# Kernel tuning notes

Measured on AMD Instinct MI355X. Metric: run time of the kernel, lower is better.

The kernel has to match this reference:

```python
import jax, jax.numpy as jnp
import numpy as np

TOP_K = 2


def setup_inputs() -> dict:
    key = jax.random.key(0)
    k0, k1, k2, k3 = jax.random.split(key, 4)
    N, D, O, E = 131072, 512, 512, 16
    H = D // 4  # gate hidden: gate_input_size // 4
    x = jax.random.normal(k0, (N, D), dtype=jnp.float32)
    # gate MLP params (task_bh=0 gate; Linear weights stored as [in, out])
    Wg1 = jax.random.normal(k1, (D, H), dtype=jnp.float32) / np.sqrt(D).astype(np.float32)
    bg1 = jnp.zeros((H,), jnp.float32)
    Wg2 = jax.random.normal(k2, (H, E), dtype=jnp.float32) * 0.02
    bg2 = jnp.zeros((E,), jnp.float32)
    # per-expert Linear(D, O) weights stacked [E, D, O]
    We = jax.random.normal(k3, (E, D, O), dtype=jnp.float32) / np.sqrt(D).astype(np.float32)
    be = jnp.zeros((E, O), jnp.float32)
    return {"x": x, "Wg1": Wg1, "bg1": bg1, "Wg2": Wg2, "bg2": bg2,
            "We": We, "be": be, "task_bh": 0}


def reference(x, Wg1, bg1, Wg2, bg2, We, be, task_bh):
    # --- top_k_gating (noisy_gating=False path) ---
    h = jax.nn.gelu(x @ Wg1 + bg1, approximate=False)  # nn.GELU default is exact erf
    logits = h @ Wg2 + bg2                              # [N, E]
    probs = jax.nn.softmax(logits, axis=1) + 1e-4       # [N, E]
    top_g, top_i = jax.lax.top_k(probs, TOP_K)          # [N, K]
    N, E = probs.shape
    # dense gate matrix: zeros.scatter(1, top_k_indices, top_k_gates)
    gates = jnp.zeros_like(probs).at[jnp.arange(N)[:, None], top_i].set(top_g)
    # --- dispatch / per-expert GEMM / combine ---
    # Equivalent to: gather tokens per expert, expert Linear, scale by gate,
    # scatter-add back. Since gates[n, e] == 0 for unselected experts, the
    # combined output equals sum_e gates[:, e] * (x @ We[e] + be[e]).
    def body(acc, ewb):
        W_e, b_e, g_e = ewb                      # [D,O], [O], [N]
        return acc + g_e[:, None] * (x @ W_e + b_e), None
    init = jnp.zeros((N, We.shape[2]), x.dtype)
    out, _ = jax.lax.scan(body, init, (We, be, gates.T))
    return out
```

## Files before the change

kernel.cpp:

```cpp
#include <hip/hip_runtime.h>
#include <cstdint>
#include <math.h>


#define NTOK 131072
#define DDIM 512
#define NT 16

typedef _Float16 f16;
typedef f16   f16x8 __attribute__((ext_vector_type(8)));
typedef float f32x4 __attribute__((ext_vector_type(4)));

__device__ __forceinline__ void load_lds16(const void* g, void* l){
  __builtin_amdgcn_global_load_lds(
      (const __attribute__((address_space(1))) void*)(uintptr_t)g,
      (__attribute__((address_space(3))) void*)(uintptr_t)l, 16, 0, 0);
}

__device__ __forceinline__ f32x4 MFMAH(f16x8 a, f16x8 b, f32x4 c){
  return __builtin_amdgcn_mfma_f32_16x16x32_f16(a, b, c, 0, 0, 0);
}

__device__ __forceinline__ f16x8 readF64h(const char* buf, int r, int q){
  return *(const f16x8*)(buf + r*128 + ((q ^ (r & 7)) << 4));
}
__device__ __forceinline__ f16x8 pack8f(const float* fv){
  f16x8 v;
  #pragma unroll
  for (int j=0;j<8;++j) v[j] = (f16)fv[j];
  return v;
}

__global__ void kconv(const float* __restrict__ Wg1, const float* __restrict__ Wg2,
                      f16* __restrict__ W1, char* __restrict__ Wg2f, int* __restrict__ ctrl){
  __shared__ float sh[64*65];
  int bx = blockIdx.x, tid = threadIdx.x;
  if (bx < 16){
    int dt = bx >> 1, ht = bx & 1;
    const float* src = Wg1 + (size_t)dt*64*128 + ht*64;
    #pragma unroll
    for (int it=0; it<16; ++it){ int idx = it*256+tid; int dl = idx>>6, ol = idx&63;
      sh[dl*65+ol] = src[dl*128+ol]; }
    __syncthreads();
    #pragma unroll
    for (int it=0; it<16; ++it){ int idx = it*256+tid; int ol = idx>>6, dl = idx&63;
      W1[(size_t)(ht*64+ol)*512 + dt*64+dl] = (f16)sh[dl*65+ol]; }
  } else {
    int ks = tid >> 6, l = tid & 63;
    int col = l & 15, kb = ks*32 + ((l >> 4) << 3);
    f16x8 v;
    #pragma unroll
    for (int j=0;j<8;++j) v[j] = (f16)Wg2[(kb+j)*16 + col];
    *(f16x8*)(Wg2f + (ks*64+l)*16) = v;
    #pragma unroll
    for (int i = 0; i < 8; ++i) ctrl[tid + i*256] = 0;
  }
}

__global__ __launch_bounds__(256) void kgate(
    const float* __restrict__ x, const f16* __restrict__ W1, const char* __restrict__ Wg2f,
    const float* __restrict__ bg1, const float* __restrict__ bg2,
    const float* __restrict__ We, f16* __restrict__ Wt,
    f16* __restrict__ xbf,
    int2* __restrict__ gate_e, float2* __restrict__ gate_g,
    int* __restrict__ refine_cnt, int* __restrict__ refine_list, int* __restrict__ counts)
{
  __shared__ __align__(16) char sm[76800];
  const int BOFF = 32768;
  const int LOGI = 67584;
  const int HIST = 75776;
  int tid = threadIdx.x, bid = blockIdx.x;
  int lane = tid & 63, w = tid >> 6, wm = w >> 1, wn = w & 1;
  int l15 = lane & 15, l4 = lane >> 4;
  int t0 = bid * 128;
  int ar = tid >> 1, ach = tid & 1;
  const float* xrow = x + (size_t)(t0 + ar) * DDIM;
  char* xbfb = (char*)xbf;
  f32x4 acc[4][4];
  #pragma unroll
  for (int n=0;n<4;++n){
    float bb = bg1[wn*64 + n*16 + l15];
    f32x4 z = {bb, bb, bb, bb};
    #pragma unroll
    for (int m=0;m<4;++m) acc[m][n] = z;
  }
  auto stageA = [&](int ks, char* abuf){
    float fv[32];
    #pragma unroll
    for (int q=0;q<8;++q) *(float4*)&fv[q*4] = *(const float4*)(xrow + ks*64 + ach*32 + q*4);
    f16x8 h0 = pack8f(fv), h1 = pack8f(fv+8), h2 = pack8f(fv+16), h3 = pack8f(fv+24);
    *(f16x8*)(abuf + ar*128 + (((ach*4+0) ^ (ar & 7)) << 4)) = h0;
    *(f16x8*)(abuf + ar*128 + (((ach*4+1) ^ (ar & 7)) << 4)) = h1;
    *(f16x8*)(abuf + ar*128 + (((ach*4+2) ^ (ar & 7)) << 4)) = h2;
    *(f16x8*)(abuf + ar*128 + (((ach*4+3) ^ (ar & 7)) << 4)) = h3;
    if (xbf){
      char* xd = xbfb + (size_t)(t0+ar)*1024 + ks*128 + ach*64;
      *(f16x8*)xd = h0; *(f16x8*)(xd+16) = h1; *(f16x8*)(xd+32) = h2; *(f16x8*)(xd+48) = h3;
    }
  };
  auto stageB = [&](int ks, char* lds){
    const char* gb = (const char*)W1 + ks*128;
    #pragma unroll
    for (int i = 0; i < 4; ++i){
      int lin = i*4096 + tid*16;
      int r = lin >> 7, g = (lin >> 4) & 7;
      load_lds16(gb + r*1024 + ((g ^ (r & 7)) << 4), lds + i*4096 + ((tid >> 6) << 10));
    }
  };
  stageB(0, sm + BOFF); stageA(0, sm);
  for (int ks = 0; ks < 8; ++ks){
    int b = ks & 1;
    asm volatile("s_waitcnt vmcnt(0)" ::: "memory");
    __syncthreads();
    if (ks < 7) stageB(ks+1, sm + BOFF + (b^1)*16384);
    const char* Ab = sm + b*16384;
    const char* Bb = sm + BOFF + b*16384;
    f16x8 ah[4][2], bh[4][2];
    #pragma unroll
    for (int m=0;m<4;++m)
      #pragma unroll
      for (int kf=0;kf<2;++kf) ah[m][kf] = readF64h(Ab, wm*64 + m*16 + l15, kf*4 + l4);
    #pragma unroll
    for (int n=0;n<4;++n)
      #pragma unroll
      for (int kf=0;kf<2;++kf) bh[n][kf] = readF64h(Bb, wn*64 + n*16 + l15, kf*4 + l4);
    #pragma unroll
    for (int m=0;m<4;++m)
      #pragma unroll
      for (int n=0;n<4;++n){
        acc[m][n] = MFMAH(ah[m][0], bh[n][0], acc[m][n]);
        acc[m][n] = MFMAH(ah[m][1], bh[n][1], acc[m][n]);
      }
    if (ks < 7) stageA(ks+1, sm + (b^1)*16384);
  }
  __syncthreads();
  uint4 wgf[4];
  #pragma unroll
  for (int ksq=0; ksq<4; ++ksq) wgf[ksq] = *(const uint4*)(Wg2f + (ksq*64+lane)*16);
  float* hl = (float*)sm;
  #pragma unroll
  for (int m=0;m<4;++m)
    #pragma unroll
    for (int n=0;n<4;++n)
      #pragma unroll
      for (int j=0;j<4;++j){
        int row = wm*64 + m*16 + (l4 << 2) + j;
        int col = wn*64 + n*16 + l15;
        float uv = acc[m][n][j];
        hl[row*132 + col] = 0.5f * uv * (1.0f + erff(uv * 0.70710678118654752f));
      }
  __syncthreads();
  {
    float bb2 = bg2[l15];
    float* ll = (float*)(sm + LOGI);
    #pragma unroll
    for (int sub=0; sub<2; ++sub){
      f32x4 acc2 = {bb2, bb2, bb2, bb2};
      #pragma unroll
      for (int ksq=0; ksq<4; ++ksq){
        const float* hp = (const float*)sm + (w*32 + sub*16 + l15)*132 + ksq*32 + l4*8;
        f16x8 afr;
        #pragma unroll
        for (int j=0;j<8;++j) afr[j] = (f16)hp[j];
        acc2 = MFMAH(afr, *(const f16x8*)&wgf[ksq], acc2);
      }
      #pragma unroll
      for (int j=0;j<4;++j) ll[(w*32 + sub*16 + l4*4 + j)*16 + l15] = acc2[j];
    }
  }
  int* hist = (int*)(sm + HIST);
  hist[tid] = 0;
  __syncthreads();
  if (tid < 128){
    int t = t0 + tid;
    const float* l = (const float*)(sm + LOGI) + tid*16;
    float b1 = -1e30f, b2 = -1e30f, b3 = -1e30f; int e1 = 0, e2 = 0;
    #pragma unroll
    for (int e = 0; e < 16; ++e){
      float v = l[e];
      if (v > b1){ b3 = b2; b2 = b1; e2 = e1; b1 = v; e1 = e; }
      else if (v > b2){ b3 = b2; b2 = v; e2 = e; }
      else if (v > b3){ b3 = v; }
    }
    float s = 0.f;
    #pragma unroll
    for (int e = 0; e < 16; ++e) s += expf(l[e] - b1);
    float inv = 1.f / s;
    gate_e[t] = make_int2(e1, e2);
    gate_g[t] = make_float2(inv + 1e-4f, expf(b2 - b1) * inv + 1e-4f);
    if (b2 - b3 < 1e-3f){
      int pos = atomicAdd(refine_cnt, 1);
      refine_list[pos] = t;
    }
    int pa = min(e1, e2), pb = max(e1, e2);
    atomicAdd(&hist[pa*16 + pb], 1);
  }
  __syncthreads();
  if (hist[tid]) atomicAdd(&counts[tid], hist[tid]);
  __syncthreads();
  {
    float* sh = (float*)sm;
    int e = bid >> 6, dt = (bid >> 3) & 7, ot = bid & 7;
    const float* src = We + (size_t)e*262144 + (size_t)dt*64*512 + ot*64;
    #pragma unroll
    for (int it=0; it<16; ++it){ int idx = it*256+tid; int dl = idx>>6, ol = idx&63;
      sh[dl*65+ol] = src[dl*512+ol]; }
    __syncthreads();
    f16* dst = Wt + (size_t)e*262144 + (size_t)ot*64*512 + dt*64;
    #pragma unroll
    for (int it=0; it<16; ++it){ int idx = it*256+tid; int ol = idx>>6, dl = idx&63;
      dst[(size_t)ol*512+dl] = (f16)sh[dl*65+ol]; }
  }
}

__global__ __launch_bounds__(128) void krefine(
    const float* __restrict__ x, const float* __restrict__ Wg1, const float* __restrict__ bg1,
    const float* __restrict__ Wg2, const float* __restrict__ bg2,
    const int* __restrict__ refine_cnt, const int* __restrict__ refine_list,
    int2* __restrict__ gate_e, float2* __restrict__ gate_g, int* __restrict__ counts)
{
  __shared__ float  xs[512];
  __shared__ double hd[128];
  __shared__ double ld[16];
  int tid = threadIdx.x;
  int rc = *refine_cnt;
  for (int i = blockIdx.x; i < rc; i += gridDim.x){
    __syncthreads();
    int t = refine_list[i];
    *(float4*)(xs + tid*4) = *(const float4*)(x + (size_t)t*DDIM + tid*4);
    __syncthreads();
    double a0=0.0, a1=0.0, a2=0.0, a3=0.0;
    for (int d = 0; d < 512; d += 4){
      a0 += (double)xs[d]   * (double)Wg1[(d)*128 + tid];
      a1 += (double)xs[d+1] * (double)Wg1[(d+1)*128 + tid];
      a2 += (double)xs[d+2] * (double)Wg1[(d+2)*128 + tid];
      a3 += (double)xs[d+3] * (double)Wg1[(d+3)*128 + tid];
    }
    double a = (double)bg1[tid] + ((a0+a1)+(a2+a3));
    hd[tid] = 0.5 * a * (1.0 + erf(a * 0.70710678118654752440));
    __syncthreads();
    if (tid < 16){
      double s0=0.0, s1=0.0;
      for (int k = 0; k < 128; k += 2){
        s0 += hd[k]   * (double)Wg2[(k)*16 + tid];
        s1 += hd[k+1] * (double)Wg2[(k+1)*16 + tid];
      }
      ld[tid] = (double)bg2[tid] + s0 + s1;
    }
    __syncthreads();
    if (tid == 0){
      int2 olde = gate_e[t];
      double b1 = -1e300, b2 = -1e300; int e1 = 0, e2 = 0;
      for (int e = 0; e < 16; ++e){
        double v = ld[e];
        if (v > b1){ b2 = b1; e2 = e1; b1 = v; e1 = e; }
        else if (v > b2){ b2 = v; e2 = e; }
      }
      double s = 0.0;
      for (int e = 0; e < 16; ++e) s += exp(ld[e] - b1);
      double inv = 1.0 / s;
      int oldp = min(olde.x, olde.y)*16 + max(olde.x, olde.y);
      int newp = min(e1, e2)*16 + max(e1, e2);
      if (oldp != newp){ atomicSub(&counts[oldp], 1); atomicAdd(&counts[newp], 1); }
      gate_e[t] = make_int2(e1, e2);
      gate_g[t] = make_float2((float)(inv + 1e-4), (float)(exp(b2 - b1) * inv + 1e-4));
    }
  }
}

__global__ __launch_bounds__(256) void kscatter(
    const int2* __restrict__ gate_e, const float2* __restrict__ gate_g,
    const int* __restrict__ counts,
    int* __restrict__ bases, int* __restrict__ cursors,
    int* __restrict__ tile_pair, int* __restrict__ tile_row0, int* __restrict__ ntiles,
    int* __restrict__ pair_tok, float2* __restrict__ pair_g, int ts)
{
  __shared__ int h[256];
  __shared__ int gb[256];
  __shared__ int bl[257];
  int tid = threadIdx.x;
  h[tid] = 0;
  if (tid < 64){
    int l = tid;
    int4 c = *(const int4*)(counts + l*4);
    int s = c.x + c.y + c.z + c.w;
    int ps = s;
    #pragma unroll
    for (int d = 1; d < 64; d <<= 1){ int v = __shfl_up(ps, d); if (l >= d) ps += v; }
    int ex = ps - s;
    bl[4*l+0] = ex;
    bl[4*l+1] = ex + c.x;
    bl[4*l+2] = ex + c.x + c.y;
    bl[4*l+3] = ex + c.x + c.y + c.z;
    if (l == 63) bl[256] = ex + s;
    if (blockIdx.x == 0){
      *(int4*)(bases + 4*l) = make_int4(bl[4*l], bl[4*l+1], bl[4*l+2], bl[4*l+3]);
      if (l == 63) bases[256] = ex + s;
      int t0 = (c.x + ts-1)/ts, t1 = (c.y + ts-1)/ts, t2 = (c.z + ts-1)/ts, t3 = (c.w + ts-1)/ts;
      int tsum = t0 + t1 + t2 + t3;
      int pt = tsum;
      #pragma unroll
      for (int d = 1; d < 64; d <<= 1){ int v = __shfl_up(pt, d); if (l >= d) pt += v; }
      int ext = pt - tsum;
      if (l == 63) *ntiles = ext + tsum;
      int tb = ext;
      int cc[4] = {c.x, c.y, c.z, c.w};
      #pragma unroll
      for (int j = 0; j < 4; ++j){
        int pp = 4*l + j;
        for (int r = 0; r < cc[j]; r += ts){ tile_pair[tb] = pp; tile_row0[tb] = r; ++tb; }
      }
    }
  }
  __syncthreads();
  int t = blockIdx.x*256 + tid;
  int2 ee = gate_e[t]; float2 gg = gate_g[t];
  int a, b; float ga, gbv;
  if (ee.x < ee.y){ a = ee.x; b = ee.y; ga = gg.x; gbv = gg.y; }
  else            { a = ee.y; b = ee.x; ga = gg.y; gbv = gg.x; }
  int p = a*16 + b;
  int off = atomicAdd(&h[p], 1);
  __syncthreads();
  if (h[tid]) gb[tid] = bl[tid] + atomicAdd(&cursors[tid], h[tid]);
  __syncthreads();
  int slot = gb[p] + off;
  pair_tok[slot] = t;
  pair_g[slot] = make_float2(ga, gbv);
}

#define SB0 __builtin_amdgcn_sched_barrier(0)
#define PH_MID do{ __builtin_amdgcn_s_barrier(); \
                   asm volatile("s_waitcnt lgkmcnt(0)"); SB0; }while(0)
#define PH_END do{ SB0; __builtin_amdgcn_s_barrier(); }while(0)

#define RDA(hp, mb) do{ \
  _Pragma("unroll") for (int m_=0;m_<4;++m_){ \
    int r_ = ((mb)+m_)*16 + l15; \
    af[m_][0] = readF64h(hp, r_, l4); \
    af[m_][1] = readF64h(hp, r_, 4+l4); }}while(0)
#define RDB4(hp) do{ \
  _Pragma("unroll") for (int n_=0;n_<4;++n_){ \
    int r_ = bln + n_*16 + l15; \
    bb[n_][0] = readF64h(hp, r_, l4); \
    bb[n_][1] = readF64h(hp, r_, 4+l4); }}while(0)
#define MMAC32(mb) do{ \
  __builtin_amdgcn_s_setprio(1); \
  _Pragma("unroll") for (int m_=0;m_<4;++m_){ \
    _Pragma("unroll") for (int n_=0;n_<4;++n_){ \
      acc[(mb)+m_][n_] = MFMAH(af[m_][0], bb[n_][0], acc[(mb)+m_][n_]); \
      acc[(mb)+m_][n_] = MFMAH(af[m_][1], bb[n_][1], acc[(mb)+m_][n_]); }} \
  __builtin_amdgcn_s_setprio(0); \
}while(0)

__global__ __launch_bounds__(512, 2) void kexpert2(
    const f16* __restrict__ xbf, const f16* __restrict__ Wt, const float* __restrict__ be,
    float* __restrict__ out,
    const int* __restrict__ counts, const int* __restrict__ bases,
    const int* __restrict__ tile_pair, const int* __restrict__ tile_row0, const int* __restrict__ ntiles,
    const int* __restrict__ pair_tok, const float2* __restrict__ pair_g)
{
  __shared__ __align__(16) char sm[134144];
  const int BBASE = 65536, LTOK = 131072, LG = 132096;
  int bid = blockIdx.x;
  int tile = ((bid >> 4) << 3) | (bid & 7);
  int nt = (bid >> 3) & 1;
  if (tile >= *ntiles) return;
  int p = tile_pair[tile], row0 = tile_row0[tile];
  int base = bases[p], cnt = counts[p];
  int eA = p >> 4, eB = p & 15;
  int tid = threadIdx.x, lane = tid & 63, w = tid >> 6;
  int wm = w >> 2, wn = w & 3;
  int l15 = lane & 15, l4 = lane >> 4;
  int bln = (wn & 1) * 64;
  if (tid < 256){
    int rr = row0 + tid; bool v = rr < cnt;
    ((int*)(sm + LTOK))[tid] = v ? pair_tok[base + rr] : -1;
    ((float2*)(sm + LG))[tid] = v ? pair_g[base + rr] : make_float2(0.f, 1.f);
  }
  __syncthreads();

  int rr0 = tid >> 3;
  int sw = ((tid & 7) ^ (rr0 & 7)) << 4;
  const char* xb = (const char*)xbf;
  const char* srcA[2][2];
  #pragma unroll
  for (int h = 0; h < 2; ++h)
    #pragma unroll
    for (int i = 0; i < 2; ++i){
      int tk = ((const int*)(sm + LTOK))[h*128 + i*64 + rr0];
      if (tk < 0) tk = 0;
      srcA[h][i] = xb + (size_t)tk*1024 + sw;
    }
  const char* srcB0 = (const char*)Wt + (size_t)eA*524288 + (size_t)(nt*256 + rr0)*1024 + sw;
  long long edelt = ((long long)eB - eA) * 524288;
  char* dA = sm + w*1024;
  char* dB = sm + BBASE + w*1024;

  auto stA = [&](int t, int h){
    if (t >= NT) return;
    int ks = t & 7, bf_ = t & 1;
    load_lds16(srcA[h][0] + ks*128, dA + bf_*32768 + h*16384);
    load_lds16(srcA[h][1] + ks*128, dA + bf_*32768 + h*16384 + 8192);
  };
  auto stB = [&](int t, int h){
    if (t >= NT) return;
    int ks = t & 7, bf_ = t & 1;
    long long eo = ((t >= 8) ? edelt : 0) + ks*128;
    load_lds16(srcB0 + h*131072 + eo,         dB + bf_*32768 + h*16384);
    load_lds16(srcB0 + h*131072 + 65536 + eo, dB + bf_*32768 + h*16384 + 8192);
  };

  const char* A0 = sm + wm*16384;
  const char* A1 = A0 + 32768;
  const char* B0 = sm + BBASE + (wn >> 1)*16384;
  const char* B1 = B0 + 32768;

  f32x4 acc[8][4];
  #pragma unroll
  for (int m = 0; m < 8; ++m)
    #pragma unroll
    for (int n = 0; n < 4; ++n) acc[m][n] = (f32x4){0.f,0.f,0.f,0.f};

  stA(0,0); stA(0,1); stB(0,0); stB(0,1); stB(1,0); stB(1,1);
  asm volatile("s_waitcnt vmcnt(4)"); SB0;
  __builtin_amdgcn_s_barrier();

  f16x8 af[4][2], bb[4][2];
  #pragma unroll 1
  for (int i = 0; i < 8; ++i){
    int t0 = 2*i, t1 = t0 + 1;
    RDA(A0, 0); RDB4(B0); stA(t1, 0); stA(t1, 1);
    PH_MID; MMAC32(0); PH_END;
    RDA(A0, 4); stB(t0+2, 0); stB(t0+2, 1);
    if (i != 7) { asm volatile("s_waitcnt vmcnt(4)"); SB0; }
    else        { asm volatile("s_waitcnt vmcnt(0)"); SB0; }
    PH_MID; MMAC32(4); PH_END;
    RDA(A1, 0); RDB4(B1); stA(t0+2, 0); stA(t0+2, 1);
    PH_MID; MMAC32(0); PH_END;
    RDA(A1, 4); stB(t1+2, 0); stB(t1+2, 1);
    if (i != 7) { asm volatile("s_waitcnt vmcnt(4)"); SB0; }
    PH_MID; MMAC32(4); PH_END;
    if (i == 3){
      #pragma unroll
      for (int m = 0; m < 8; ++m)
        #pragma unroll
        for (int j = 0; j < 4; ++j){
          int row = wm*128 + m*16 + l4*4 + j;
          float2 g2 = ((const float2*)(sm + LG))[row];
          float r_ = g2.x / g2.y;
          #pragma unroll
          for (int n = 0; n < 4; ++n) acc[m][n][j] *= r_;
        }
    }
  }

  float bcA[4], bcB[4];
  #pragma unroll
  for (int n = 0; n < 4; ++n){
    int col = nt*256 + wn*64 + n*16 + l15;
    bcA[n] = be[(size_t)eA*DDIM + col];
    bcB[n] = be[(size_t)eB*DDIM + col];
  }
  #pragma unroll
  for (int m = 0; m < 8; ++m)
    #pragma unroll
    for (int j = 0; j < 4; ++j){
      int row = wm*128 + m*16 + l4*4 + j;
      int tk = ((const int*)(sm + LTOK))[row];
      if (tk >= 0){
        float2 g2 = ((const float2*)(sm + LG))[row];
        float* orow = out + (size_t)tk*DDIM + nt*256 + wn*64;
        #pragma unroll
        for (int n = 0; n < 4; ++n)
          orow[n*16 + l15] = g2.y*acc[m][n][j] + g2.x*bcA[n] + g2.y*bcB[n];
      }
    }
}

__global__ __launch_bounds__(256, 2) void kexpertF(
    const float* __restrict__ x,
    const f16* __restrict__ Wt, const float* __restrict__ be,
    float* __restrict__ out,
    const int* __restrict__ counts, const int* __restrict__ bases,
    const int* __restrict__ tile_pair, const int* __restrict__ tile_row0, const int* __restrict__ ntiles,
    const int* __restrict__ pair_tok, const float2* __restrict__ pair_g)
{
  __shared__ __align__(16) char sm[67072];
  const int ABUF = 0, BBUF = 32768, LTOK = 65536, LGOFF = 66048;
  int tile = blockIdx.x >> 2, nt = blockIdx.x & 3;
  if (tile >= *ntiles) return;
  int p = tile_pair[tile], row0 = tile_row0[tile];
  int base = bases[p], cnt = counts[p];
  int eA = p >> 4, eB = p & 15;
  int tid = threadIdx.x, lane = tid & 63;
  int w = tid >> 6, wm = w >> 1, wn = w & 1;
  if (tid < 128){
    int rr = row0 + tid; bool v = rr < cnt;
    ((int*)(sm + LTOK))[tid] = v ? pair_tok[base + rr] : -1;
    ((float2*)(sm + LGOFF))[tid] = v ? pair_g[base + rr] : make_float2(0.f, 0.f);
  }
  __syncthreads();
  const char* wb = (const char*)Wt;
  int grp = tid >> 3, gch = tid & 7;
  int swz = (gch ^ (grp & 7)) << 4;
  long long edelt = ((long long)eB - (long long)eA) * 524288;
  const char* srcB[4];
  #pragma unroll
  for (int i = 0; i < 4; ++i)
    srcB[i] = wb + (long long)eA*524288 + (size_t)(nt*128 + i*32 + grp)*1024 + swz;
  int arow = tid >> 1, ach = tid & 1;
  int tkr = ((const int*)(sm + LTOK))[arow];
  if (tkr < 0) tkr = 0;
  const float* xrow = x + (size_t)tkr*DDIM + ach*32;
  int ldst = (w << 10);
  #pragma unroll
  for (int i = 0; i < 4; ++i) load_lds16(srcB[i], sm + BBUF + i*4096 + ldst);
  {
    #pragma unroll
    for (int q2 = 0; q2 < 4; ++q2){
      float fv[8];
      *(float4*)&fv[0] = *(const float4*)(xrow + q2*8);
      *(float4*)&fv[4] = *(const float4*)(xrow + q2*8 + 4);
      f16x8 hv = pack8f(fv);
      int g = ach*4 + q2;
      *(f16x8*)(sm + ABUF + arow*128 + ((g ^ (arow & 7)) << 4)) = hv;
    }
  }
  f32x4 acc[4][4], res[4][4];
  #pragma unroll
  for (int m=0;m<4;++m)
    #pragma unroll
    for (int n=0;n<4;++n) acc[m][n] = (f32x4){0.f,0.f,0.f,0.f};
  for (int u = 0; u < 16; ++u){
    int b = u & 1;
    asm volatile("s_waitcnt vmcnt(0)" ::: "memory");
    __syncthreads();
    int un = u + 1;
    f16x8 hv[4];
    if (un < 16){
      int b2 = un & 1;
      long long aoff = (long long)(un & 7) * 128;
      long long boff = aoff + ((un >> 3) ? edelt : 0);
      #pragma unroll
      for (int i = 0; i < 4; ++i)
        load_lds16(srcB[i] + boff, sm + BBUF + b2*16384 + i*4096 + ldst);
      const float* xr = xrow + (un & 7)*64;
      #pragma unroll
      for (int q2 = 0; q2 < 4; ++q2){
        float fv[8];
        *(float4*)&fv[0] = *(const float4*)(xr + q2*8);
        *(float4*)&fv[4] = *(const float4*)(xr + q2*8 + 4);
        hv[q2] = pack8f(fv);
      }
    }
    const char* Ab = sm + ABUF + b*16384;
    const char* Bb = sm + BBUF + b*16384;
    f16x8 af2[4][2], bf2[4][2];
    #pragma unroll
    for (int m=0;m<4;++m){
      int r = wm*64 + m*16 + (lane & 15);
      af2[m][0] = readF64h(Ab, r, (lane >> 4));
      af2[m][1] = readF64h(Ab, r, 4 + (lane >> 4));
    }
    #pragma unroll
    for (int n=0;n<4;++n){
      int r = wn*64 + n*16 + (lane & 15);
      bf2[n][0] = readF64h(Bb, r, (lane >> 4));
      bf2[n][1] = readF64h(Bb, r, 4 + (lane >> 4));
    }
    #pragma unroll
    for (int m=0;m<4;++m)
      #pragma unroll
      for (int n=0;n<4;++n){
        acc[m][n] = MFMAH(af2[m][0], bf2[n][0], acc[m][n]);
        acc[m][n] = MFMAH(af2[m][1], bf2[n][1], acc[m][n]);
      }
    if (un < 16){
      int b2 = un & 1;
      #pragma unroll
      for (int q2 = 0; q2 < 4; ++q2){
        int g = ach*4 + q2;
        *(f16x8*)(sm + ABUF + b2*16384 + arow*128 + ((g ^ (arow & 7)) << 4)) = hv[q2];
      }
    }
    if (u == 7){
      const float* bev = be + (size_t)eA*DDIM + nt*128;
      float bcol[4];
      #pragma unroll
      for (int n=0;n<4;++n) bcol[n] = bev[wn*64 + n*16 + (lane & 15)];
      #pragma unroll
      for (int m=0;m<4;++m)
        #pragma unroll
        for (int j=0;j<4;++j){
          int row = wm*64 + m*16 + ((lane >> 4) << 2) + j;
          float g = ((const float2*)(sm + LGOFF))[row].x;
          #pragma unroll
          for (int n=0;n<4;++n){
            res[m][n][j] = g * (acc[m][n][j] + bcol[n]);
            acc[m][n][j] = 0.f;
          }
        }
    }
    if (u == 15){
      const float* bev = be + (size_t)eB*DDIM + nt*128;
      float bcol[4];
      #pragma unroll
      for (int n=0;n<4;++n) bcol[n] = bev[wn*64 + n*16 + (lane & 15)];
      #pragma unroll
      for (int m=0;m<4;++m)
        #pragma unroll
        for (int j=0;j<4;++j){
          int row = wm*64 + m*16 + ((lane >> 4) << 2) + j;
          int tk = ((const int*)(sm + LTOK))[row];
          float g = ((const float2*)(sm + LGOFF))[row].y;
          if (tk >= 0){
            float* orow = out + (size_t)tk*DDIM + nt*128;
            #pragma unroll
            for (int n=0;n<4;++n)
              orow[wn*64 + n*16 + (lane & 15)] = res[m][n][j] + g * (acc[m][n][j] + bcol[n]);
          }
        }
    }
  }
}

extern "C" void kernel_launch(void* const* d_in, const int* in_sizes, int n_in,
                              void* d_out, int out_size, void* d_ws, size_t ws_size,
                              hipStream_t stream)
{
  const float* x   = (const float*)d_in[0];
  const float* Wg1 = (const float*)d_in[1];
  const float* bg1 = (const float*)d_in[2];
  const float* Wg2 = (const float*)d_in[3];
  const float* bg2 = (const float*)d_in[4];
  const float* We  = (const float*)d_in[5];
  const float* be  = (const float*)d_in[6];
  float* out = (float*)d_out;
  char* ws = (char*)d_ws;

  f16*  Wt          = (f16*)(ws + 0);
  f16*  W1          = (f16*)(ws + 8388608);
  char* Wg2f        = ws + 8519680;
  char* CTRL        = ws + 8650752;
  int*  refine_cnt  = (int*)(CTRL);
  int*  ntiles      = (int*)(CTRL + 4);
  int*  counts      = (int*)(CTRL + 64);
  int*  cursors     = (int*)(CTRL + 2048);
  int*  bases       = (int*)(CTRL + 4096);
  int2*   gate_e    = (int2*)(ws + 8658944);
  float2* gate_g    = (float2*)(ws + 9707520);
  int*  refine_list = (int*)(ws + 10756096);
  int*  pair_tok    = (int*)(ws + 11280384);
  float2* pair_g    = (float2*)(ws + 11804672);
  int*  tile_pair   = (int*)(ws + 12853248);
  int*  tile_row0   = (int*)(ws + 12863488);
  const size_t XBF_OFF = 16777216ull;
  const size_t XBF_BYTES = (size_t)NTOK * DDIM * 2;
  bool bf16a = ws_size >= XBF_OFF + XBF_BYTES;
  f16* xbf = bf16a ? (f16*)(ws + XBF_OFF) : nullptr;

  hipLaunchKernelGGL(kconv,    dim3(17),   dim3(256), 0, stream, Wg1, Wg2, W1, Wg2f,
                     (int*)CTRL);
  hipLaunchKernelGGL(kgate,    dim3(1024), dim3(256), 0, stream, x, W1, Wg2f, bg1, bg2,
                     We, Wt, xbf, gate_e, gate_g, refine_cnt, refine_list, counts);
  hipLaunchKernelGGL(krefine,  dim3(512),  dim3(128), 0, stream, x, Wg1, bg1, Wg2, bg2,
                     refine_cnt, refine_list, gate_e, gate_g, counts);
  hipLaunchKernelGGL(kscatter, dim3(512),  dim3(256), 0, stream, gate_e, gate_g, counts,
                     bases, cursors, tile_pair, tile_row0, ntiles, pair_tok, pair_g,
                     bf16a ? 256 : 128);
  if (bf16a)
    hipLaunchKernelGGL(kexpert2, dim3(1408), dim3(512), 0, stream, xbf, Wt, be, out,
                       counts, bases, tile_pair, tile_row0, ntiles, pair_tok, pair_g);
  else
    hipLaunchKernelGGL(kexpertF, dim3(5120), dim3(256), 0, stream, x, Wt, be, out,
                       counts, bases, tile_pair, tile_row0, ntiles, pair_tok, pair_g);
  (void)in_sizes; (void)n_in; (void)out_size; (void)ws_size;
}
```

Measured before the change: 461.2 us.

## Restructure expert GEMM to 256x128 tiles with triple-buffered 32-wide K steps

Replaces the expert GEMM kernel with a version that computes 256x128 output tiles instead of 256x256 and splits N into four parts. It uses 32-element K slices staged through a three-deep LDS ring. Per-block LDS drops from about 134KB to about 77KB and accumulators are halved, which allows four blocks per CU instead of two. The aim is higher occupancy and better latency hiding. In exchange the x-row gathers are repeated across four N tiles instead of two, and there are more barriers per unit of K work.

```diff
diff --git a/kernel.cpp b/kernel.cpp
--- a/kernel.cpp
+++ b/kernel.cpp
@@ -5,7 +5,6 @@
 
 #define NTOK 131072
 #define DDIM 512
-#define NT 16
 
 typedef _Float16 f16;
 typedef f16   f16x8 __attribute__((ext_vector_type(8)));
@@ -23,6 +22,9 @@
 
 __device__ __forceinline__ f16x8 readF64h(const char* buf, int r, int q){
   return *(const f16x8*)(buf + r*128 + ((q ^ (r & 7)) << 4));
+}
+__device__ __forceinline__ f16x8 readF32h(const char* buf, int r, int q){
+  return *(const f16x8*)(buf + r*64 + ((q ^ (r & 3)) << 4));
 }
 __device__ __forceinline__ f16x8 pack8f(const float* fv){
   f16x8 v;
@@ -329,49 +331,26 @@
 }
 
 #define SB0 __builtin_amdgcn_sched_barrier(0)
-#define PH_MID do{ __builtin_amdgcn_s_barrier(); \
-                   asm volatile("s_waitcnt lgkmcnt(0)"); SB0; }while(0)
-#define PH_END do{ SB0; __builtin_amdgcn_s_barrier(); }while(0)
-
-#define RDA(hp, mb) do{ \
-  _Pragma("unroll") for (int m_=0;m_<4;++m_){ \
-    int r_ = ((mb)+m_)*16 + l15; \
-    af[m_][0] = readF64h(hp, r_, l4); \
-    af[m_][1] = readF64h(hp, r_, 4+l4); }}while(0)
-#define RDB4(hp) do{ \
-  _Pragma("unroll") for (int n_=0;n_<4;++n_){ \
-    int r_ = bln + n_*16 + l15; \
-    bb[n_][0] = readF64h(hp, r_, l4); \
-    bb[n_][1] = readF64h(hp, r_, 4+l4); }}while(0)
-#define MMAC32(mb) do{ \
-  __builtin_amdgcn_s_setprio(1); \
-  _Pragma("unroll") for (int m_=0;m_<4;++m_){ \
-    _Pragma("unroll") for (int n_=0;n_<4;++n_){ \
-      acc[(mb)+m_][n_] = MFMAH(af[m_][0], bb[n_][0], acc[(mb)+m_][n_]); \
-      acc[(mb)+m_][n_] = MFMAH(af[m_][1], bb[n_][1], acc[(mb)+m_][n_]); }} \
-  __builtin_amdgcn_s_setprio(0); \
-}while(0)
-
-__global__ __launch_bounds__(512, 2) void kexpert2(
+
+__global__ __launch_bounds__(512, 4) void kexpert3(
     const f16* __restrict__ xbf, const f16* __restrict__ Wt, const float* __restrict__ be,
     float* __restrict__ out,
     const int* __restrict__ counts, const int* __restrict__ bases,
     const int* __restrict__ tile_pair, const int* __restrict__ tile_row0, const int* __restrict__ ntiles,
     const int* __restrict__ pair_tok, const float2* __restrict__ pair_g)
 {
-  __shared__ __align__(16) char sm[134144];
-  const int BBASE = 65536, LTOK = 131072, LG = 132096;
+  __shared__ __align__(16) char sm[76800];
+  const int ABASE = 0, BBASE = 49152, LTOK = 73728, LG = 74752;
   int bid = blockIdx.x;
-  int tile = ((bid >> 4) << 3) | (bid & 7);
-  int nt = (bid >> 3) & 1;
+  int tile = ((bid >> 5) << 3) | (bid & 7);
+  int nt = (bid >> 3) & 3;
   if (tile >= *ntiles) return;
   int p = tile_pair[tile], row0 = tile_row0[tile];
   int base = bases[p], cnt = counts[p];
   int eA = p >> 4, eB = p & 15;
   int tid = threadIdx.x, lane = tid & 63, w = tid >> 6;
-  int wm = w >> 2, wn = w & 3;
+  int wm = w >> 1, wn = w & 1;
   int l15 = lane & 15, l4 = lane >> 4;
-  int bln = (wn & 1) * 64;
   if (tid < 256){
     int rr = row0 + tid; bool v = rr < cnt;
     ((int*)(sm + LTOK))[tid] = v ? pair_tok[base + rr] : -1;
@@ -379,97 +358,99 @@
   }
   __syncthreads();
 
-  int rr0 = tid >> 3;
-  int sw = ((tid & 7) ^ (rr0 & 7)) << 4;
+  int rr = tid >> 2;
+  int swz = ((tid & 3) ^ (rr & 3)) << 4;
   const char* xb = (const char*)xbf;
-  const char* srcA[2][2];
-  #pragma unroll
-  for (int h = 0; h < 2; ++h)
-    #pragma unroll
-    for (int i = 0; i < 2; ++i){
-      int tk = ((const int*)(sm + LTOK))[h*128 + i*64 + rr0];
-      if (tk < 0) tk = 0;
-      srcA[h][i] = xb + (size_t)tk*1024 + sw;
-    }
-  const char* srcB0 = (const char*)Wt + (size_t)eA*524288 + (size_t)(nt*256 + rr0)*1024 + sw;
+  const char* srcA[2];
+  #pragma unroll
+  for (int i = 0; i < 2; ++i){
+    int tk = ((const int*)(sm + LTOK))[i*128 + rr];
+    if (tk < 0) tk = 0;
+    srcA[i] = xb + (size_t)tk*1024 + swz;
+  }
+  const char* srcB0 = (const char*)Wt + (size_t)eA*524288 + (size_t)(nt*128 + rr)*1024 + swz;
   long long edelt = ((long long)eB - eA) * 524288;
-  char* dA = sm + w*1024;
-  char* dB = sm + BBASE + w*1024;
-
-  auto stA = [&](int t, int h){
-    if (t >= NT) return;
-    int ks = t & 7, bf_ = t & 1;
-    load_lds16(srcA[h][0] + ks*128, dA + bf_*32768 + h*16384);
-    load_lds16(srcA[h][1] + ks*128, dA + bf_*32768 + h*16384 + 8192);
+  int wbase = w*1024;
+
+  auto stA = [&](int t, int bf_){
+    if (t >= 32) return;
+    int ks = t & 15;
+    load_lds16(srcA[0] + ks*64, sm + ABASE + bf_*16384 + wbase);
+    load_lds16(srcA[1] + ks*64, sm + ABASE + bf_*16384 + 8192 + wbase);
   };
-  auto stB = [&](int t, int h){
-    if (t >= NT) return;
-    int ks = t & 7, bf_ = t & 1;
-    long long eo = ((t >= 8) ? edelt : 0) + ks*128;
-    load_lds16(srcB0 + h*131072 + eo,         dB + bf_*32768 + h*16384);
-    load_lds16(srcB0 + h*131072 + 65536 + eo, dB + bf_*32768 + h*16384 + 8192);
+  auto stB = [&](int t, int bf_){
+    if (t >= 32) return;
+    int ks = t & 15;
+    long long eo = ((t >= 16) ? edelt : 0) + ks*64;
+    load_lds16(srcB0 + eo, sm + BBASE + bf_*8192 + wbase);
   };
 
-  const char* A0 = sm + wm*16384;
-  const char* A1 = A0 + 32768;
-  const char* B0 = sm + BBASE + (wn >> 1)*16384;
-  const char* B1 = B0 + 32768;
-
-  f32x4 acc[8][4];
-  #pragma unroll
-  for (int m = 0; m < 8; ++m)
+  f32x4 acc[4][4];
+  #pragma unroll
+  for (int m = 0; m < 4; ++m)
     #pragma unroll
     for (int n = 0; n < 4; ++n) acc[m][n] = (f32x4){0.f,0.f,0.f,0.f};
 
-  stA(0,0); stA(0,1); stB(0,0); stB(0,1); stB(1,0); stB(1,1);
-  asm volatile("s_waitcnt vmcnt(4)"); SB0;
+  stA(0, 0); stB(0, 0); stA(1, 1); stB(1, 1);
+  asm volatile("s_waitcnt vmcnt(3)"); SB0;
   __builtin_amdgcn_s_barrier();
 
-  f16x8 af[4][2], bb[4][2];
+  int bcur = 0, bstg = 2;
+  f16x8 af[4], bb[4];
   #pragma unroll 1
-  for (int i = 0; i < 8; ++i){
-    int t0 = 2*i, t1 = t0 + 1;
-    RDA(A0, 0); RDB4(B0); stA(t1, 0); stA(t1, 1);
-    PH_MID; MMAC32(0); PH_END;
-    RDA(A0, 4); stB(t0+2, 0); stB(t0+2, 1);
-    if (i != 7) { asm volatile("s_waitcnt vmcnt(4)"); SB0; }
-    else        { asm volatile("s_waitcnt vmcnt(0)"); SB0; }
-    PH_MID; MMAC32(4); PH_END;
-    RDA(A1, 0); RDB4(B1); stA(t0+2, 0); stA(t0+2, 1);
-    PH_MID; MMAC32(0); PH_END;
-    RDA(A1, 4); stB(t1+2, 0); stB(t1+2, 1);
-    if (i != 7) { asm volatile("s_waitcnt vmcnt(4)"); SB0; }
-    PH_MID; MMAC32(4); PH_END;
-    if (i == 3){
-      #pragma unroll
-      for (int m = 0; m < 8; ++m)
+  for (int t = 0; t < 32; ++t){
+    const char* Ab = sm + ABASE + bcur*16384;
+    const char* Bb = sm + BBASE + bcur*8192;
+    #pragma unroll
+    for (int m = 0; m < 4; ++m) af[m] = readF32h(Ab, wm*64 + m*16 + l15, l4);
+    #pragma unroll
+    for (int n = 0; n < 4; ++n) bb[n] = readF32h(Bb, wn*64 + n*16 + l15, l4);
+    stA(t+2, bstg); stB(t+2, bstg);
+    if (t < 30)       { asm volatile("s_waitcnt vmcnt(3)"); SB0; }
+    else if (t == 30) { asm volatile("s_waitcnt vmcnt(0)"); SB0; }
+    __builtin_amdgcn_s_barrier();
+    asm volatile("s_waitcnt lgkmcnt(0)"); SB0;
+    __builtin_amdgcn_s_setprio(1);
+    #pragma unroll
+    for (int m = 0; m < 4; ++m)
+      #pragma unroll
+      for (int n = 0; n < 4; ++n)
+        acc[m][n] = MFMAH(af[m], bb[n], acc[m][n]);
+    __builtin_amdgcn_s_setprio(0);
+    SB0;
+    __builtin_amdgcn_s_barrier();
+    if (t == 15){
+      #pragma unroll
+      for (int m = 0; m < 4; ++m)
         #pragma unroll
         for (int j = 0; j < 4; ++j){
-          int row = wm*128 + m*16 + l4*4 + j;
+          int row = wm*64 + m*16 + l4*4 + j;
           float2 g2 = ((const float2*)(sm + LG))[row];
           float r_ = g2.x / g2.y;
           #pragma unroll
           for (int n = 0; n < 4; ++n) acc[m][n][j] *= r_;
         }
     }
+    bcur = (bcur == 2) ? 0 : bcur + 1;
+    bstg = (bstg == 2) ? 0 : bstg + 1;
   }
 
   float bcA[4], bcB[4];
   #pragma unroll
   for (int n = 0; n < 4; ++n){
-    int col = nt*256 + wn*64 + n*16 + l15;
+    int col = nt*128 + wn*64 + n*16 + l15;
     bcA[n] = be[(size_t)eA*DDIM + col];
     bcB[n] = be[(size_t)eB*DDIM + col];
   }
   #pragma unroll
-  for (int m = 0; m < 8; ++m)
+  for (int m = 0; m < 4; ++m)
     #pragma unroll
     for (int j = 0; j < 4; ++j){
-      int row = wm*128 + m*16 + l4*4 + j;
+      int row = wm*64 + m*16 + l4*4 + j;
       int tk = ((const int*)(sm + LTOK))[row];
       if (tk >= 0){
         float2 g2 = ((const float2*)(sm + LG))[row];
-        float* orow = out + (size_t)tk*DDIM + nt*256 + wn*64;
+        float* orow = out + (size_t)tk*DDIM + nt*128 + wn*64;
         #pragma unroll
         for (int n = 0; n < 4; ++n)
           orow[n*16 + l15] = g2.y*acc[m][n][j] + g2.x*bcA[n] + g2.y*bcB[n];
@@ -669,7 +650,7 @@
                      bases, cursors, tile_pair, tile_row0, ntiles, pair_tok, pair_g,
                      bf16a ? 256 : 128);
   if (bf16a)
-    hipLaunchKernelGGL(kexpert2, dim3(1408), dim3(512), 0, stream, xbf, Wt, be, out,
+    hipLaunchKernelGGL(kexpert3, dim3(2816), dim3(512), 0, stream, xbf, Wt, be, out,
                        counts, bases, tile_pair, tile_row0, ntiles, pair_tok, pair_g);
   else
     hipLaunchKernelGGL(kexpertF, dim3(5120), dim3(256), 0, stream, x, Wt, be, out,
```

After: 468.6 us. About the same (+1.6%).
